# Performance work log

Measured on AMD Instinct MI355X. Metric: run time of the kernel, lower is better.

The kernel has to match this reference:

```python
import jax, jax.numpy as jnp
import numpy as np

STRIDE, PADDING, EPS = 2, 1, 1e-5


def setup_inputs() -> dict:
    key = jax.random.key(0)
    k1, k2, k3 = jax.random.split(key, 3)
    C_in, C_out, K = 64, 64, 4
    x = jax.random.normal(k1, (32, C_in, 64, 64), dtype=jnp.float32)
    weight = jax.random.normal(k2, (C_in, C_out, K, K), dtype=jnp.float32) * 0.05  # torch layout (in,out,kh,kw)
    conv_bias = jax.random.normal(k3, (C_out,), dtype=jnp.float32) * 0.02
    gamma = jnp.ones((C_out,), dtype=jnp.float32)
    beta = jnp.zeros((C_out,), dtype=jnp.float32)
    running_mean = jnp.zeros((C_out,), dtype=jnp.float32)
    running_var = jnp.ones((C_out,), dtype=jnp.float32)
    return {"x": x, "weight": weight, "conv_bias": conv_bias, "gamma": gamma,
            "beta": beta, "running_mean": running_mean, "running_var": running_var}


def _conv_transpose2d(x, weight, bias, stride, padding):
    # torch.nn.functional.conv_transpose2d equivalent:
    # conv with lhs_dilation=stride, spatially-flipped kernel, in/out axes swapped,
    # and padding k-1-p on each side.
    k = weight.shape[2]
    w_t = jnp.transpose(jnp.flip(weight, (2, 3)), (1, 0, 2, 3))  # (Cout, Cin, k, k)
    pad = k - 1 - padding
    y = jax.lax.conv_general_dilated(
        x, w_t,
        window_strides=(1, 1),
        padding=[(pad, pad), (pad, pad)],
        lhs_dilation=(stride, stride),
        dimension_numbers=("NCHW", "OIHW", "NCHW"),
    )
    return y + bias[None, :, None, None]


def reference(x, weight, conv_bias, gamma, beta, running_mean, running_var):
    # ConvTranspose2d
    y = _conv_transpose2d(x, weight, conv_bias, STRIDE, PADDING)  # [N,C,128,128]
    # BatchNorm2d (inference, running stats)
    scale = gamma * jax.lax.rsqrt(running_var + EPS)
    y = (y - running_mean[None, :, None, None]) * scale[None, :, None, None] + beta[None, :, None, None]
    # Softmax over channel dim
    y = jax.nn.softmax(y, axis=1)
    # MaxPool2d(k=2, s=2): H,W are even, so reshape-max is exact
    N, C, H, W = y.shape
    y = y.reshape(N, C, H // 2, 2, W // 2, 2).max(axis=(3, 5))  # [N,C,64,64]
    return y
```

## Files before the change

kernel.cpp:

```cpp
#include <hip/hip_runtime.h>
#include <hip/hip_bf16.h>
#include <math.h>


typedef __attribute__((ext_vector_type(8))) short short8;
typedef __attribute__((ext_vector_type(4))) float floatx4;
typedef __attribute__((ext_vector_type(2))) unsigned uint2v;

__device__ ushort g_wfrag[4 * 8 * 4 * 64 * 8];
__device__ float g_aff[64];

#define L2E 1.44269504088896340736f

__device__ __forceinline__ ushort f2bf(float f) {
  union { float f; unsigned u; } v; v.f = f;
  unsigned r = v.u + 0x7FFF + ((v.u >> 16) & 1);
  return (ushort)(r >> 16);
}

__global__ __launch_bounds__(256) void prep_kernel(
    const float* __restrict__ w, const float* __restrict__ bias,
    const float* __restrict__ gamma, const float* __restrict__ beta,
    const float* __restrict__ mean, const float* __restrict__ var) {
  int t = blockIdx.x * 256 + threadIdx.x;
  int cin0 = (t >> 6) * 2;
  int cout = t & 63;
  int nt = cout >> 4, b15 = cout & 15;
  int q = (cin0 & 31) >> 3;
  int j = cin0 & 7;
  int ksq = cin0 >> 5;
  float Aw = gamma[cout] * rsqrtf(var[cout] + 1e-5f) * L2E;

  const float4* p0 = (const float4*)&w[(cin0 * 64 + cout) * 16];
  const float4* p1 = (const float4*)&w[((cin0 + 1) * 64 + cout) * 16];
  float a[16], b[16];
  {
    float4 f0 = p0[0], f1 = p0[1], f2 = p0[2], f3 = p0[3];
    a[0]=f0.x; a[1]=f0.y; a[2]=f0.z; a[3]=f0.w; a[4]=f1.x; a[5]=f1.y; a[6]=f1.z; a[7]=f1.w;
    a[8]=f2.x; a[9]=f2.y; a[10]=f2.z; a[11]=f2.w; a[12]=f3.x; a[13]=f3.y; a[14]=f3.z; a[15]=f3.w;
    float4 g0 = p1[0], g1 = p1[1], g2 = p1[2], g3 = p1[3];
    b[0]=g0.x; b[1]=g0.y; b[2]=g0.z; b[3]=g0.w; b[4]=g1.x; b[5]=g1.y; b[6]=g1.z; b[7]=g1.w;
    b[8]=g2.x; b[9]=g2.y; b[10]=g2.z; b[11]=g2.w; b[12]=g3.x; b[13]=g3.y; b[14]=g3.z; b[15]=g3.w;
  }
#pragma unroll
  for (int kh = 0; kh < 4; ++kh)
#pragma unroll
    for (int kw = 0; kw < 4; ++kw) {
      int r = (kh & 1) ? 0 : 1;
      int pp = (kw & 1) ? 0 : 1;
      int c = r * 2 + pp;
      int tap = (kh >> 1) * 2 + (kw >> 1);
      int ks = tap * 2 + ksq;
      unsigned u = (unsigned)f2bf(a[kh * 4 + kw] * Aw) |
                   ((unsigned)f2bf(b[kh * 4 + kw] * Aw) << 16);
      *(unsigned*)&g_wfrag[(((c * 8 + ks) * 4 + nt) * 64 + q * 16 + b15) * 8 + j] = u;
    }

  if (t < 64) {
    float A0 = gamma[t] * rsqrtf(var[t] + 1e-5f);
    g_aff[t] = ((bias[t] - mean[t]) * A0 + beta[t]) * L2E;
  }
}

__device__ __forceinline__ unsigned cvtpk(float a, float b) {
  unsigned r;
  asm("v_cvt_pk_bf16_f32 %0, %1, %2" : "=v"(r) : "v"(a), "v"(b));
  return r;
}

template <int CTRL>
__device__ __forceinline__ float dpp_add(float v) {
  unsigned t = (unsigned)__builtin_amdgcn_update_dpp(
      0, (int)__float_as_uint(v), CTRL, 0xF, 0xF, true);
  return v + __uint_as_float(t);
}

__device__ __forceinline__ float sum16(float v) {
  v = dpp_add<0xB1>(v);
  v = dpp_add<0x4E>(v);
  v = dpp_add<0x141>(v);
  v = dpp_add<0x140>(v);
  return v;
}

__device__ __forceinline__ float fexp2(float x) {
#if __has_builtin(__builtin_amdgcn_exp2f)
  return __builtin_amdgcn_exp2f(x);
#else
  return exp2f(x);
#endif
}

__device__ __forceinline__ void gload_lds16(const void* g, void* l) {
  __builtin_amdgcn_global_load_lds(
      (const __attribute__((address_space(1))) void*)g,
      (__attribute__((address_space(3))) void*)l, 16, 0, 0);
}

#define COLS 66
#define ROWSTRIDE (COLS * 64)

__global__ __launch_bounds__(512, 4) void fused_kernel(const float* __restrict__ x,
                                                       float* __restrict__ out) {
  __shared__ __align__(16) ushort xs[4 * ROWSTRIDE];
  __shared__ __align__(16) ushort wbuf[2 * 16 * 512];

  const int tid  = threadIdx.x;
  const int swz  = ((blockIdx.x & 7) << 2) | (blockIdx.x >> 3);
  const int ph0  = swz * 2;
  const int n    = blockIdx.y;
  const int wave = tid >> 6;
  const int lane = tid & 63;
  const int b15  = lane & 15;
  const int q    = lane >> 4;
  const int wc   = wave & 1;
  const int c    = wave >> 1;
  const int r    = c >> 1, p = c & 1;

#define STAGE_W(buf_, ksrc_)                                                      \
  {                                                                               \
    const int nt0_ = 2 * wc;                                                      \
    gload_lds16(&g_wfrag[(((c * 8 + (ksrc_)) * 4 + nt0_) * 64 + lane) * 8],       \
                &wbuf[((buf_) * 16 + c * 4 + nt0_) * 512]);                       \
    gload_lds16(&g_wfrag[(((c * 8 + (ksrc_)) * 4 + nt0_ + 1) * 64 + lane) * 8],   \
                &wbuf[((buf_) * 16 + c * 4 + nt0_ + 1) * 512]);                   \
  }
  STAGE_W(0, 0);

  for (int e = tid; e < 1024; e += 512) {
    int iw4 = e & 15;
    int c4  = (e >> 4) & 15;
    int row = e >> 8;
    int ih  = ph0 - 1 + row;
    float4 v0 = {0.f, 0.f, 0.f, 0.f}, v1 = v0, v2 = v0, v3 = v0;
    if (ih >= 0 && ih < 64) {
      const float* xp = x + ((n * 64 + c4 * 4) * 64 + ih) * 64 + iw4 * 4;
      v0 = *(const float4*)xp;          v1 = *(const float4*)(xp + 4096);
      v2 = *(const float4*)(xp + 8192); v3 = *(const float4*)(xp + 12288);
    }
    int chunk = c4 >> 1, half4 = (c4 & 1) * 4;
    float cc[4][4] = {{v0.x, v1.x, v2.x, v3.x}, {v0.y, v1.y, v2.y, v3.y},
                      {v0.z, v1.z, v2.z, v3.z}, {v0.w, v1.w, v2.w, v3.w}};
#pragma unroll
    for (int ii = 0; ii < 4; ++ii) {
      int col = iw4 * 4 + ii + 1;
      uint2v pk = {cvtpk(cc[ii][0], cc[ii][1]), cvtpk(cc[ii][2], cc[ii][3])};
      *(uint2v*)&xs[(row * COLS + col) * 64 + ((chunk ^ (col & 7)) * 8) + half4] = pk;
    }
  }
  for (int e = tid; e < 128; e += 512) {
    int c4 = e & 15, side = (e >> 4) & 1, row = e >> 5;
    int col = side ? 65 : 0;
    int chunk = c4 >> 1, half4 = (c4 & 1) * 4;
    ushort4 z; z.x = z.y = z.z = z.w = 0;
    *(ushort4*)&xs[(row * COLS + col) * 64 + ((chunk ^ (col & 7)) * 8) + half4] = z;
  }

  float Dc[4];
#pragma unroll
  for (int nt = 0; nt < 4; ++nt) Dc[nt] = g_aff[nt * 16 + b15];

  int A_[2][2][2];
#pragma unroll
  for (int mt = 0; mt < 2; ++mt)
#pragma unroll
    for (int b = 0; b < 2; ++b) {
      int col = wc * 32 + mt * 16 + b15 + (b ? p - 1 : p) + 1;
#pragma unroll
      for (int par = 0; par < 2; ++par)
        A_[mt][b][par] = r * ROWSTRIDE + col * 64 + (((par * 4 + q) ^ (col & 7)) * 8);
    }

  __syncthreads();

  floatx4 acc[16];
#pragma unroll
  for (int i = 0; i < 16; ++i) {
    float d = Dc[i & 3];
    acc[i] = (floatx4){d, d, d, d};
  }

#pragma unroll
  for (int ks = 0; ks < 8; ++ks) {
    const int cur = ks & 1;
    if (ks < 7) STAGE_W(cur ^ 1, ks + 1);
    const int b_ = (ks >> 1) & 1, par_ = ks & 1;
    const int ro = (ks >> 2) ? 0 : ROWSTRIDE;
    short8 af00 = *(const short8*)&xs[A_[0][b_][par_] + ro];
    short8 af01 = *(const short8*)&xs[A_[1][b_][par_] + ro];
    short8 af10 = *(const short8*)&xs[A_[0][b_][par_] + ro + ROWSTRIDE];
    short8 af11 = *(const short8*)&xs[A_[1][b_][par_] + ro + ROWSTRIDE];
#pragma unroll
    for (int nt = 0; nt < 4; ++nt) {
      short8 bf = *(const short8*)&wbuf[((cur * 16 + c * 4 + nt) * 64 + lane) * 8];
      acc[nt]      = __builtin_amdgcn_mfma_f32_16x16x32_bf16(af00, bf, acc[nt], 0, 0, 0);
      acc[4 + nt]  = __builtin_amdgcn_mfma_f32_16x16x32_bf16(af01, bf, acc[4 + nt], 0, 0, 0);
      acc[8 + nt]  = __builtin_amdgcn_mfma_f32_16x16x32_bf16(af10, bf, acc[8 + nt], 0, 0, 0);
      acc[12 + nt] = __builtin_amdgcn_mfma_f32_16x16x32_bf16(af11, bf, acc[12 + nt], 0, 0, 0);
    }
    __syncthreads();
  }

  float* red = (float*)xs;
  {
    float4 z = {0.f, 0.f, 0.f, 0.f};
    for (int e = tid; e < 2080; e += 512) ((float4*)red)[e] = z;
  }
  __syncthreads();

#pragma unroll
  for (int prow = 0; prow < 2; ++prow)
#pragma unroll
    for (int mt = 0; mt < 2; ++mt) {
      float sm[4] = {0.f, 0.f, 0.f, 0.f};
#pragma unroll
      for (int nt = 0; nt < 4; ++nt)
#pragma unroll
        for (int reg = 0; reg < 4; ++reg) {
          float e = fexp2(acc[prow * 8 + mt * 4 + nt][reg]);
          acc[prow * 8 + mt * 4 + nt][reg] = e;
          sm[reg] += e;
        }
#pragma unroll
      for (int reg = 0; reg < 4; ++reg)
        sm[reg] = __builtin_amdgcn_rcpf(sum16(sm[reg]));
#pragma unroll
      for (int nt = 0; nt < 4; ++nt) {
        int idx = (prow * 64 + nt * 16 + b15) * 65 + wc * 32 + mt * 16 + q * 4;
#pragma unroll
        for (int reg = 0; reg < 4; ++reg) {
          float v = acc[prow * 8 + mt * 4 + nt][reg] * sm[reg];
          __hip_atomic_fetch_max((unsigned*)&red[idx + reg], __float_as_uint(v),
                                 __ATOMIC_RELAXED, __HIP_MEMORY_SCOPE_WORKGROUP);
        }
      }
    }
  __syncthreads();

  for (int e = tid; e < 4096; e += 512) {
    int pw2  = e & 31;
    int cout = (e >> 5) & 63;
    int rl   = e >> 11;
    int base = (rl * 64 + cout) * 65 + pw2 * 2;
    float2 val = {red[base], red[base + 1]};
    *(float2*)&out[((n * 64 + cout) * 64 + (ph0 + rl)) * 64 + pw2 * 2] = val;
  }
}

extern "C" void kernel_launch(void* const* d_in, const int* in_sizes, int n_in,
                              void* d_out, int out_size, void* d_ws, size_t ws_size,
                              hipStream_t stream) {
  const float* x     = (const float*)d_in[0];
  const float* w     = (const float*)d_in[1];
  const float* bias  = (const float*)d_in[2];
  const float* gamma = (const float*)d_in[3];
  const float* beta  = (const float*)d_in[4];
  const float* mean  = (const float*)d_in[5];
  const float* var   = (const float*)d_in[6];
  float* out = (float*)d_out;

  prep_kernel<<<8, 256, 0, stream>>>(w, bias, gamma, beta, mean, var);
  dim3 grid(32, 32);
  fused_kernel<<<grid, 512, 0, stream>>>(x, out);
}
```

Baseline: 112.3 us.

## Load weight fragments directly into registers, dropping LDS staging and per-step barriers

Weight B-fragments now go from global memory straight into registers, double-buffered across the k-steps, instead of being staged into a shared-memory buffer with global_load_lds. This removes the __syncthreads after every k-step and the LDS round trip for the weights. The reduction scratch moves to its own dedicated LDS array that is zeroed up front, so the barrier after the main loop is also gone. In exchange each wave issues its own global loads, which should mostly hit in L2, and register pressure rises by 8 short8 values at 4 blocks/SM of 512 threads.

```diff
diff --git a/kernel.cpp b/kernel.cpp
--- a/kernel.cpp
+++ b/kernel.cpp
@@ -91,19 +91,13 @@
 #endif
 }
 
-__device__ __forceinline__ void gload_lds16(const void* g, void* l) {
-  __builtin_amdgcn_global_load_lds(
-      (const __attribute__((address_space(1))) void*)g,
-      (__attribute__((address_space(3))) void*)l, 16, 0, 0);
-}
-
 #define COLS 66
 #define ROWSTRIDE (COLS * 64)
 
 __global__ __launch_bounds__(512, 4) void fused_kernel(const float* __restrict__ x,
                                                        float* __restrict__ out) {
   __shared__ __align__(16) ushort xs[4 * ROWSTRIDE];
-  __shared__ __align__(16) ushort wbuf[2 * 16 * 512];
+  __shared__ __align__(16) float red[2 * 64 * 65 + 16];
 
   const int tid  = threadIdx.x;
   const int swz  = ((blockIdx.x & 7) << 2) | (blockIdx.x >> 3);
@@ -117,15 +111,17 @@
   const int c    = wave >> 1;
   const int r    = c >> 1, p = c & 1;
 
-#define STAGE_W(buf_, ksrc_)                                                      \
-  {                                                                               \
-    const int nt0_ = 2 * wc;                                                      \
-    gload_lds16(&g_wfrag[(((c * 8 + (ksrc_)) * 4 + nt0_) * 64 + lane) * 8],       \
-                &wbuf[((buf_) * 16 + c * 4 + nt0_) * 512]);                       \
-    gload_lds16(&g_wfrag[(((c * 8 + (ksrc_)) * 4 + nt0_ + 1) * 64 + lane) * 8],   \
-                &wbuf[((buf_) * 16 + c * 4 + nt0_ + 1) * 512]);                   \
-  }
-  STAGE_W(0, 0);
+  short8 bfA[4], bfB[4];
+  {
+    const short8* wf = (const short8*)g_wfrag + (c * 8) * 256;
+#pragma unroll
+    for (int nt = 0; nt < 4; ++nt) bfA[nt] = wf[nt * 64 + lane];
+  }
+
+  {
+    float4 z = {0.f, 0.f, 0.f, 0.f};
+    for (int e = tid; e < 2084; e += 512) ((float4*)red)[e] = z;
+  }
 
   for (int e = tid; e < 1024; e += 512) {
     int iw4 = e & 15;
@@ -160,16 +156,14 @@
 #pragma unroll
   for (int nt = 0; nt < 4; ++nt) Dc[nt] = g_aff[nt * 16 + b15];
 
-  int A_[2][2][2];
-#pragma unroll
-  for (int mt = 0; mt < 2; ++mt)
-#pragma unroll
-    for (int b = 0; b < 2; ++b) {
-      int col = wc * 32 + mt * 16 + b15 + (b ? p - 1 : p) + 1;
-#pragma unroll
-      for (int par = 0; par < 2; ++par)
-        A_[mt][b][par] = r * ROWSTRIDE + col * 64 + (((par * 4 + q) ^ (col & 7)) * 8);
-    }
+  int A2[2][2];
+#pragma unroll
+  for (int b = 0; b < 2; ++b) {
+    int col = wc * 32 + b15 + (b ? p - 1 : p) + 1;
+#pragma unroll
+    for (int par = 0; par < 2; ++par)
+      A2[b][par] = r * ROWSTRIDE + col * 64 + (((par * 4 + q) ^ (col & 7)) * 8);
+  }
 
   __syncthreads();
 
@@ -182,31 +176,28 @@
 
 #pragma unroll
   for (int ks = 0; ks < 8; ++ks) {
-    const int cur = ks & 1;
-    if (ks < 7) STAGE_W(cur ^ 1, ks + 1);
+    short8* bcur = (ks & 1) ? bfB : bfA;
+    short8* bnxt = (ks & 1) ? bfA : bfB;
+    if (ks < 7) {
+      const short8* wf = (const short8*)g_wfrag + (c * 8 + ks + 1) * 256;
+#pragma unroll
+      for (int nt = 0; nt < 4; ++nt) bnxt[nt] = wf[nt * 64 + lane];
+    }
     const int b_ = (ks >> 1) & 1, par_ = ks & 1;
     const int ro = (ks >> 2) ? 0 : ROWSTRIDE;
-    short8 af00 = *(const short8*)&xs[A_[0][b_][par_] + ro];
-    short8 af01 = *(const short8*)&xs[A_[1][b_][par_] + ro];
-    short8 af10 = *(const short8*)&xs[A_[0][b_][par_] + ro + ROWSTRIDE];
-    short8 af11 = *(const short8*)&xs[A_[1][b_][par_] + ro + ROWSTRIDE];
+    const int base = A2[b_][par_] + ro;
+    short8 af00 = *(const short8*)&xs[base];
+    short8 af01 = *(const short8*)&xs[base + 1024];
+    short8 af10 = *(const short8*)&xs[base + ROWSTRIDE];
+    short8 af11 = *(const short8*)&xs[base + ROWSTRIDE + 1024];
 #pragma unroll
     for (int nt = 0; nt < 4; ++nt) {
-      short8 bf = *(const short8*)&wbuf[((cur * 16 + c * 4 + nt) * 64 + lane) * 8];
-      acc[nt]      = __builtin_amdgcn_mfma_f32_16x16x32_bf16(af00, bf, acc[nt], 0, 0, 0);
-      acc[4 + nt]  = __builtin_amdgcn_mfma_f32_16x16x32_bf16(af01, bf, acc[4 + nt], 0, 0, 0);
-      acc[8 + nt]  = __builtin_amdgcn_mfma_f32_16x16x32_bf16(af10, bf, acc[8 + nt], 0, 0, 0);
-      acc[12 + nt] = __builtin_amdgcn_mfma_f32_16x16x32_bf16(af11, bf, acc[12 + nt], 0, 0, 0);
-    }
-    __syncthreads();
-  }
-
-  float* red = (float*)xs;
-  {
-    float4 z = {0.f, 0.f, 0.f, 0.f};
-    for (int e = tid; e < 2080; e += 512) ((float4*)red)[e] = z;
-  }
-  __syncthreads();
+      acc[nt]      = __builtin_amdgcn_mfma_f32_16x16x32_bf16(af00, bcur[nt], acc[nt], 0, 0, 0);
+      acc[4 + nt]  = __builtin_amdgcn_mfma_f32_16x16x32_bf16(af01, bcur[nt], acc[4 + nt], 0, 0, 0);
+      acc[8 + nt]  = __builtin_amdgcn_mfma_f32_16x16x32_bf16(af10, bcur[nt], acc[8 + nt], 0, 0, 0);
+      acc[12 + nt] = __builtin_amdgcn_mfma_f32_16x16x32_bf16(af11, bcur[nt], acc[12 + nt], 0, 0, 0);
+    }
+  }
 
 #pragma unroll
   for (int prow = 0; prow < 2; ++prow)
```

Result: slower. 124.9 us (+11.2%).
